# Optimization experiments

Hardware: AMD Instinct MI355X
Metric: run time of the kernel (lower is better)

Reference implementation:

```python
import jax, jax.numpy as jnp
import numpy as np
from jax import lax

NUM_MASKS = 100
NUM_CLASSES = 81  # 80 + 1
KERNEL_DIM = 256
BIAS_PRIOR = float(-np.log((1 - 0.01) / 0.01))


def setup_inputs() -> dict:
    key = jax.random.key(0)
    ks = jax.random.split(key, 12)
    B, C, H, W = 4, 256, 160, 160
    D = C  # expand_dim = in_channels * num_groups
    inp = {
        "features": jax.random.normal(ks[0], (B, C, H, W), jnp.float32),
        # iam_conv: Conv2d(C, num_masks, 3, padding=1)
        "w_iam": jax.random.normal(ks[1], (NUM_MASKS, C, 3, 3), jnp.float32) * 0.01,
        "b_iam": jnp.full((NUM_MASKS,), BIAS_PRIOR, jnp.float32),
        "softmax_bias": jnp.ones((1,), jnp.float32),
        # fc: Linear(D, D), xavier-ish
        "w_fc": jax.random.normal(ks[2], (D, D), jnp.float32) * (1.0 / np.sqrt(D)),
        "b_fc": jnp.zeros((D,), jnp.float32),
        "w_cls": jax.random.normal(ks[3], (NUM_CLASSES, D), jnp.float32) * 0.01,
        "b_cls": jnp.full((NUM_CLASSES,), BIAS_PRIOR, jnp.float32),
        "w_ker": jax.random.normal(ks[4], (KERNEL_DIM, D), jnp.float32) * 0.01,
        "b_ker": jnp.zeros((KERNEL_DIM,), jnp.float32),
        "w_obj": jax.random.normal(ks[5], (1, D), jnp.float32) * (1.0 / np.sqrt(D)),
        "b_obj": jnp.zeros((1,), jnp.float32),
        "w_box": jax.random.normal(ks[6], (4, D), jnp.float32) * 0.01,
        "b_box": jnp.zeros((4,), jnp.float32),
    }
    return inp


def reference(features, w_iam, b_iam, softmax_bias, w_fc, b_fc,
              w_cls, b_cls, w_ker, b_ker, w_obj, b_obj, w_box, b_box):
    B, C, H, W = features.shape
    # conv score map: (B, num_masks, H, W)
    iam = lax.conv_general_dilated(
        features, w_iam, window_strides=(1, 1), padding="SAME",
        dimension_numbers=("NCHW", "OIHW", "NCHW")) + b_iam[None, :, None, None]
    # num_groups == 1: single group iam
    iam_flat = iam.reshape(B, NUM_MASKS, H * W)
    # softmax over HW with learned scalar bias (bias shifts uniformly -> no-op math-wise but kept faithful)
    iam_prob = jax.nn.softmax(iam_flat + softmax_bias[0], axis=-1)  # (B, M, HW)
    # spatial attention pooling: bmm(prob, feats^T) -> (B, M, C)
    inst = jnp.einsum("bmp,bcp->bmc", iam_prob, features.reshape(B, C, H * W))
    # prev_inst_features is None -> skip fc_fuse
    inst = jax.nn.relu(inst @ w_fc.T + b_fc)
    pred_logits = inst @ w_cls.T + b_cls
    pred_kernel = inst @ w_ker.T + b_ker
    pred_scores = inst @ w_obj.T + b_obj
    pred_bboxes = inst @ w_box.T + b_box
    return (pred_logits, pred_kernel, pred_scores, pred_bboxes, iam, inst)
```

## Files before the change

kernel.cpp:

```cpp
#include <hip/hip_runtime.h>
#include <hip/hip_bf16.h>

typedef __attribute__((ext_vector_type(8))) short bf16x8;
typedef __attribute__((ext_vector_type(4))) float f32x4;

#define HW_ 25600
#define HP_ 162
#define WP_ 162

__device__ __forceinline__ unsigned short f2bf(float f) {
    union { float f; unsigned u; } x; x.f = f;
    unsigned r = x.u + 0x7FFFu + ((x.u >> 16) & 1u);
    return (unsigned short)(r >> 16);
}

typedef const __attribute__((address_space(1))) unsigned int* gas_t;
typedef __attribute__((address_space(3))) unsigned int* las_t;
__device__ __forceinline__ void gl_lds16(const void* g, void* l) {
    __builtin_amdgcn_global_load_lds((gas_t)g, (las_t)l, 16, 0, 0);
}

__global__ __launch_bounds__(256) void k_prepw(const float* __restrict__ w_iam,
                                               unsigned short* __restrict__ wp) {
    int idx = blockIdx.x * 256 + threadIdx.x;
    if (idx >= 36 * 8192) return;
    int stage = idx >> 13;
    int r8 = idx & 8191;
    int m = r8 >> 6, cl = r8 & 63;
    int tap = stage >> 2, cc = stage & 3;
    int c = cc * 64 + cl;
    int dy = tap / 3, dx = tap - dy * 3;
    float v = (m < 100) ? w_iam[((m * 256 + c) * 3 + dy) * 3 + dx] : 0.f;
    wp[idx] = f2bf(v);
}

__global__ __launch_bounds__(256) void k_border(unsigned short* __restrict__ fpad) {
    int idx = blockIdx.x * 256 + threadIdx.x;
    const int perb = 164864;
    if (idx >= 4 * perb) return;
    int b = idx / perb;
    int r = idx - b * perb;
    int hp, wpp, c;
    if (r < 82944) {
        hp = (r < 41472) ? 0 : 161;
        int r2 = r % 41472;
        wpp = r2 >> 8; c = r2 & 255;
    } else {
        r -= 82944;
        wpp = (r < 40960) ? 0 : 161;
        int r2 = r % 40960;
        hp = 1 + (r2 >> 8); c = r2 & 255;
    }
    fpad[((b * HP_ + hp) * WP_ + wpp) * 256 + c] = 0;
}

__global__ __launch_bounds__(256) void k_convert(const float* __restrict__ feat,
                                                 unsigned short* __restrict__ fpad) {
    int bid = blockIdx.x;
    int b = bid / 640;
    int h = (bid >> 2) % 160;
    int c0 = (bid & 3) * 64;
    __shared__ float tile[64][161];
    int t = threadIdx.x;
    const float* src = feat + ((long)(b * 256 + c0) * 160 + h) * 160;
    for (int s = 0; s < 40; ++s) {
        int q = t + s * 256;
        int ci = q / 160;
        int w = q - ci * 160;
        tile[ci][w] = src[(long)ci * HW_ + w];
    }
    __syncthreads();
    int co = (t & 7) * 8, wq = t >> 3;
    unsigned short* dst = fpad + ((long)(b * HP_ + h + 1) * WP_ + 1) * 256 + c0 + co;
    for (int wp = 0; wp < 5; ++wp) {
        int w = wq + wp * 32;
        bf16x8 v;
        #pragma unroll
        for (int j = 0; j < 8; ++j) v[j] = (short)f2bf(tile[co + j][w]);
        *(bf16x8*)(dst + (long)w * 256) = v;
    }
}

__global__ __launch_bounds__(256, 4) void k_conv(const unsigned short* __restrict__ fpad,
                                                 const unsigned short* __restrict__ wprep,
                                                 const float* __restrict__ b_iam,
                                                 float* __restrict__ iam) {
    int bid = blockIdx.x;
    bid = (bid & 7) * 100 + (bid >> 3);
    int b = bid / 200;
    int p0 = (bid % 200) * 128;
    int tid = threadIdx.x;
    int lane = tid & 63, wid = tid >> 6;

    __shared__ __align__(16) unsigned short As[128 * 64];
    __shared__ __align__(16) unsigned short Bs[128 * 64];

    const unsigned short* fb = fpad + (long)b * HP_ * WP_ * 256;
    const unsigned short* gB[4];
    #pragma unroll
    for (int rnd = 0; rnd < 4; ++rnd) {
        int r = (tid >> 3) + rnd * 32;
        int p = p0 + r;
        int h = p / 160, w = p - h * 160;
        gB[rnd] = fb + ((long)h * WP_ + w) * 256 + (tid & 7) * 8;
    }

    f32x4 acc[7][2];
    #pragma unroll
    for (int i = 0; i < 7; ++i)
        #pragma unroll
        for (int j = 0; j < 2; ++j)
            #pragma unroll
            for (int k = 0; k < 4; ++k) acc[i][j][k] = 0.f;

    int kgrp = (lane >> 4) << 3;
    int arow = lane & 15;

    for (int tap = 0; tap < 9; ++tap) {
        int dy = tap / 3, dx = tap - dy * 3;
        long toff = ((long)dy * WP_ + dx) * 256;
        #pragma unroll
        for (int cc = 0; cc < 4; ++cc) {
            int stage = tap * 4 + cc;
            const unsigned short* ga = wprep + (long)stage * 8192 + (tid << 3);
            long boff = toff + cc * 64;
            #pragma unroll
            for (int rnd = 0; rnd < 4; ++rnd) {
                gl_lds16(ga + rnd * 2048, (char*)As + (wid << 10) + (rnd << 12));
                gl_lds16(gB[rnd] + boff, (char*)Bs + (wid << 10) + (rnd << 12));
            }
            __syncthreads();
            #pragma unroll
            for (int kk = 0; kk < 64; kk += 32) {
                bf16x8 af[7], bfv[2];
                #pragma unroll
                for (int mf = 0; mf < 7; ++mf)
                    af[mf] = *(const bf16x8*)(As + (mf * 16 + arow) * 64 + kk + kgrp);
                #pragma unroll
                for (int nf = 0; nf < 2; ++nf)
                    bfv[nf] = *(const bf16x8*)(Bs + (wid * 32 + nf * 16 + arow) * 64 + kk + kgrp);
                #pragma unroll
                for (int mf = 0; mf < 7; ++mf)
                    #pragma unroll
                    for (int nf = 0; nf < 2; ++nf)
                        acc[mf][nf] = __builtin_amdgcn_mfma_f32_16x16x32_bf16(
                            af[mf], bfv[nf], acc[mf][nf], 0, 0, 0);
            }
            __syncthreads();
        }
    }
    float* dst = iam + (long)b * 100 * HW_;
    #pragma unroll
    for (int mf = 0; mf < 7; ++mf)
        #pragma unroll
        for (int nf = 0; nf < 2; ++nf) {
            int p = p0 + wid * 32 + nf * 16 + (lane & 15);
            int m0 = mf * 16 + ((lane >> 4) << 2);
            #pragma unroll
            for (int j = 0; j < 4; ++j) {
                int m = m0 + j;
                if (m < 100) dst[(long)m * HW_ + p] = acc[mf][nf][j] + b_iam[m];
            }
        }
}

__global__ __launch_bounds__(256, 2) void k_pool(const float* __restrict__ feat,
                                                 const float* __restrict__ iam,
                                                 float* __restrict__ partials,
                                                 float* __restrict__ psum) {
    int bid = blockIdx.x;
    int b = bid / 50;
    int slice = bid - b * 50;
    int p0 = slice * 512;
    int tid = threadIdx.x, lane = tid & 63, wq = tid >> 6;

    __shared__ __align__(16) unsigned short A[128 * 72];
    __shared__ __align__(16) unsigned short Bl[256 * 72];
    __shared__ float sums[128];
    if (tid < 128) sums[tid] = 0.f;
    __syncthreads();

    f32x4 acc[7][4];
    #pragma unroll
    for (int i = 0; i < 7; ++i)
        #pragma unroll
        for (int j = 0; j < 4; ++j)
            #pragma unroll
            for (int k = 0; k < 4; ++k) acc[i][j][k] = 0.f;

    int kgrp = (lane >> 4) << 3;

    for (int ks = 0; ks < 8; ++ks) {
        int k0 = p0 + ks * 64;
        for (int s = 0; s < 4; ++s) {
            int q = tid + s * 256;
            int mi = q >> 3, j0 = (q & 7) * 8;
            bf16x8 o;
            if (mi < 100) {
                const float4* sp4 = (const float4*)(iam + (long)(b * 100 + mi) * HW_ + k0 + j0);
                float4 v0 = sp4[0], v1 = sp4[1];
                float xv[8] = {v0.x, v0.y, v0.z, v0.w, v1.x, v1.y, v1.z, v1.w};
                float ls = 0.f;
                #pragma unroll
                for (int j = 0; j < 8; ++j) {
                    float e = __expf(xv[j]);
                    o[j] = (short)f2bf(e);
                    ls += e;
                }
                atomicAdd(&sums[mi], ls);
            } else {
                #pragma unroll
                for (int j = 0; j < 8; ++j) o[j] = 0;
            }
            *(bf16x8*)(A + mi * 72 + j0) = o;
        }
        for (int s = 0; s < 8; ++s) {
            int q = tid + s * 256;
            int ci = q >> 3, j0 = (q & 7) * 8;
            const float4* sp4 = (const float4*)(feat + (long)(b * 256 + ci) * HW_ + k0 + j0);
            float4 v0 = sp4[0], v1 = sp4[1];
            float xv[8] = {v0.x, v0.y, v0.z, v0.w, v1.x, v1.y, v1.z, v1.w};
            bf16x8 o;
            #pragma unroll
            for (int j = 0; j < 8; ++j) o[j] = (short)f2bf(xv[j]);
            *(bf16x8*)(Bl + ci * 72 + j0) = o;
        }
        __syncthreads();
        #pragma unroll
        for (int kk = 0; kk < 64; kk += 32) {
            bf16x8 af[7], bfv[4];
            #pragma unroll
            for (int mf = 0; mf < 7; ++mf)
                af[mf] = *(const bf16x8*)(A + (mf * 16 + (lane & 15)) * 72 + kk + kgrp);
            #pragma unroll
            for (int nf = 0; nf < 4; ++nf)
                bfv[nf] = *(const bf16x8*)(Bl + (wq * 64 + nf * 16 + (lane & 15)) * 72 + kk + kgrp);
            #pragma unroll
            for (int mf = 0; mf < 7; ++mf)
                #pragma unroll
                for (int nf = 0; nf < 4; ++nf)
                    acc[mf][nf] = __builtin_amdgcn_mfma_f32_16x16x32_bf16(
                        af[mf], bfv[nf], acc[mf][nf], 0, 0, 0);
        }
        __syncthreads();
    }
    if (tid < 100) psum[(long)(b * 50 + slice) * 112 + tid] = sums[tid];
    float* dst = partials + (long)(b * 50 + slice) * 112 * 256;
    #pragma unroll
    for (int mf = 0; mf < 7; ++mf)
        #pragma unroll
        for (int nf = 0; nf < 4; ++nf) {
            int m0 = mf * 16 + ((lane >> 4) << 2);
            int c  = wq * 64 + nf * 16 + (lane & 15);
            #pragma unroll
            for (int j = 0; j < 4; ++j)
                dst[(long)(m0 + j) * 256 + c] = acc[mf][nf][j];
        }
}

__global__ __launch_bounds__(256) void k_redpool(const float* __restrict__ partials,
                                                 const float* __restrict__ psum,
                                                 float* __restrict__ inst_pool) {
    int bid = blockIdx.x;
    int b = bid / 100, m = bid - b * 100;
    int c = threadIdx.x;
    float s = 0.f, d = 0.f;
    for (int sl = 0; sl < 50; ++sl) {
        s += partials[((long)(b * 50 + sl) * 112 + m) * 256 + c];
        d += psum[(long)(b * 50 + sl) * 112 + m];
    }
    inst_pool[(long)bid * 256 + c] = s / d;
}

__global__ __launch_bounds__(256) void k_fc(const float* __restrict__ inst_pool,
                                            const float* __restrict__ w_fc, const float* __restrict__ b_fc,
                                            const float* __restrict__ w_cls, const float* __restrict__ b_cls,
                                            const float* __restrict__ w_ker, const float* __restrict__ b_ker,
                                            const float* __restrict__ w_obj, const float* __restrict__ b_obj,
                                            const float* __restrict__ w_box, const float* __restrict__ b_box,
                                            float* __restrict__ out) {
    int r = blockIdx.x;
    int t = threadIdx.x;
    __shared__ float row[256];
    __shared__ float inst_s[256];
    row[t] = inst_pool[(long)r * 256 + t];
    __syncthreads();
    {
        float acc = b_fc[t];
        const float4* wv = (const float4*)(w_fc + (long)t * 256);
        for (int c = 0; c < 64; ++c) {
            float4 w4 = wv[c];
            acc += w4.x * row[c * 4] + w4.y * row[c * 4 + 1] + w4.z * row[c * 4 + 2] + w4.w * row[c * 4 + 3];
        }
        acc = fmaxf(acc, 0.f);
        inst_s[t] = acc;
        out[10376800 + (long)r * 256 + t] = acc;
    }
    __syncthreads();
    {
        float acc = b_ker[t];
        const float4* wv = (const float4*)(w_ker + (long)t * 256);
        for (int c = 0; c < 64; ++c) {
            float4 w4 = wv[c];
            acc += w4.x * inst_s[c * 4] + w4.y * inst_s[c * 4 + 1] + w4.z * inst_s[c * 4 + 2] + w4.w * inst_s[c * 4 + 3];
        }
        out[32400 + (long)r * 256 + t] = acc;
    }
    if (t < 81) {
        float acc = b_cls[t];
        const float4* wv = (const float4*)(w_cls + (long)t * 256);
        for (int c = 0; c < 64; ++c) {
            float4 w4 = wv[c];
            acc += w4.x * inst_s[c * 4] + w4.y * inst_s[c * 4 + 1] + w4.z * inst_s[c * 4 + 2] + w4.w * inst_s[c * 4 + 3];
        }
        out[(long)r * 81 + t] = acc;
    }
    if (t == 0) {
        float acc = b_obj[0];
        for (int c = 0; c < 256; ++c) acc += w_obj[c] * inst_s[c];
        out[134800 + r] = acc;
    }
    if (t >= 1 && t < 5) {
        int j = t - 1;
        float acc = b_box[j];
        for (int c = 0; c < 256; ++c) acc += w_box[j * 256 + c] * inst_s[c];
        out[135200 + (long)r * 4 + j] = acc;
    }
}

extern "C" void kernel_launch(void* const* d_in, const int* in_sizes, int n_in,
                              void* d_out, int out_size, void* d_ws, size_t ws_size,
                              hipStream_t stream) {
    const float* feat  = (const float*)d_in[0];
    const float* w_iam = (const float*)d_in[1];
    const float* b_iam = (const float*)d_in[2];
    const float* w_fc  = (const float*)d_in[4];
    const float* b_fc  = (const float*)d_in[5];
    const float* w_cls = (const float*)d_in[6];
    const float* b_cls = (const float*)d_in[7];
    const float* w_ker = (const float*)d_in[8];
    const float* b_ker = (const float*)d_in[9];
    const float* w_obj = (const float*)d_in[10];
    const float* b_obj = (const float*)d_in[11];
    const float* w_box = (const float*)d_in[12];
    const float* b_box = (const float*)d_in[13];
    float* out = (float*)d_out;

    char* ws = (char*)d_ws;
    unsigned short* fpad  = (unsigned short*)ws;
    unsigned short* wprep = (unsigned short*)(ws + 53747712);
    float* partials  = (float*)ws;
    float* psum      = (float*)(ws + 22937600);
    float* inst_pool = (float*)(ws + 23027200);

    float* iam = out + 136800;

    k_prepw  <<<dim3(1152), dim3(256), 0, stream>>>(w_iam, wprep);
    k_border <<<dim3(2576), dim3(256), 0, stream>>>(fpad);
    k_convert<<<dim3(2560), dim3(256), 0, stream>>>(feat, fpad);
    k_conv   <<<dim3(800),  dim3(256), 0, stream>>>(fpad, wprep, b_iam, iam);
    k_pool   <<<dim3(200),  dim3(256), 0, stream>>>(feat, iam, partials, psum);
    k_redpool<<<dim3(400),  dim3(256), 0, stream>>>(partials, psum, inst_pool);
    k_fc     <<<dim3(400),  dim3(256), 0, stream>>>(inst_pool, w_fc, b_fc, w_cls, b_cls,
                                                    w_ker, b_ker, w_obj, b_obj, w_box, b_box, out);
}
```

Measured before the change: 205.2 us.

## Double-buffer conv LDS stages and XOR-swizzle K chunks to avoid bank conflicts

The implicit-GEMM conv kernel gets two LDS buffers for A and B, so the async global_load_lds of stage s+2 is issued while stage s is computed, with explicit vmcnt waits and barriers. The weight prep and the feature-load addressing also XOR-swizzle 8-element channel groups by row, so the MFMA fragment reads from LDS avoid bank conflicts. LDS use doubles to 64KB per block and the occupancy hint of 4 blocks per CU is dropped, which lowers occupancy. The pipeline also relies on a hand-written vmcnt count being correct.

```diff
diff --git a/kernel.cpp b/kernel.cpp
--- a/kernel.cpp
+++ b/kernel.cpp
@@ -28,7 +28,8 @@
     int r8 = idx & 8191;
     int m = r8 >> 6, cl = r8 & 63;
     int tap = stage >> 2, cc = stage & 3;
-    int c = cc * 64 + cl;
+    int jj = (cl >> 3) ^ (m & 7);
+    int c = cc * 64 + jj * 8 + (cl & 7);
     int dy = tap / 3, dx = tap - dy * 3;
     float v = (m < 100) ? w_iam[((m * 256 + c) * 3 + dy) * 3 + dx] : 0.f;
     wp[idx] = f2bf(v);
@@ -81,10 +82,10 @@
     }
 }
 
-__global__ __launch_bounds__(256, 4) void k_conv(const unsigned short* __restrict__ fpad,
-                                                 const unsigned short* __restrict__ wprep,
-                                                 const float* __restrict__ b_iam,
-                                                 float* __restrict__ iam) {
+__global__ __launch_bounds__(256) void k_conv(const unsigned short* __restrict__ fpad,
+                                              const unsigned short* __restrict__ wprep,
+                                              const float* __restrict__ b_iam,
+                                              float* __restrict__ iam) {
     int bid = blockIdx.x;
     bid = (bid & 7) * 100 + (bid >> 3);
     int b = bid / 200;
@@ -92,18 +93,20 @@
     int tid = threadIdx.x;
     int lane = tid & 63, wid = tid >> 6;
 
-    __shared__ __align__(16) unsigned short As[128 * 64];
-    __shared__ __align__(16) unsigned short Bs[128 * 64];
+    __shared__ __align__(16) unsigned short As[2][8192];
+    __shared__ __align__(16) unsigned short Bs[2][8192];
 
     const unsigned short* fb = fpad + (long)b * HP_ * WP_ * 256;
     const unsigned short* gB[4];
+    int csw = (((tid & 7) ^ ((tid >> 3) & 7)) << 3);
     #pragma unroll
     for (int rnd = 0; rnd < 4; ++rnd) {
         int r = (tid >> 3) + rnd * 32;
         int p = p0 + r;
         int h = p / 160, w = p - h * 160;
-        gB[rnd] = fb + ((long)h * WP_ + w) * 256 + (tid & 7) * 8;
-    }
+        gB[rnd] = fb + ((long)h * WP_ + w) * 256 + csw;
+    }
+    const unsigned short* gA0 = wprep + (tid << 3);
 
     f32x4 acc[7][2];
     #pragma unroll
@@ -113,42 +116,65 @@
             #pragma unroll
             for (int k = 0; k < 4; ++k) acc[i][j][k] = 0.f;
 
-    int kgrp = (lane >> 4) << 3;
     int arow = lane & 15;
-
-    for (int tap = 0; tap < 9; ++tap) {
+    int cs0 = ((((lane >> 4) ^ (lane & 7))) << 3);
+    int cs1 = cs0 ^ 32;
+
+    auto issue = [&](int s, int bi) {
+        int tap = s >> 2, cc = s & 3;
         int dy = tap / 3, dx = tap - dy * 3;
-        long toff = ((long)dy * WP_ + dx) * 256;
-        #pragma unroll
-        for (int cc = 0; cc < 4; ++cc) {
-            int stage = tap * 4 + cc;
-            const unsigned short* ga = wprep + (long)stage * 8192 + (tid << 3);
-            long boff = toff + cc * 64;
-            #pragma unroll
-            for (int rnd = 0; rnd < 4; ++rnd) {
-                gl_lds16(ga + rnd * 2048, (char*)As + (wid << 10) + (rnd << 12));
-                gl_lds16(gB[rnd] + boff, (char*)Bs + (wid << 10) + (rnd << 12));
-            }
-            __syncthreads();
-            #pragma unroll
-            for (int kk = 0; kk < 64; kk += 32) {
-                bf16x8 af[7], bfv[2];
-                #pragma unroll
-                for (int mf = 0; mf < 7; ++mf)
-                    af[mf] = *(const bf16x8*)(As + (mf * 16 + arow) * 64 + kk + kgrp);
+        long boff = ((long)dy * WP_ + dx) * 256 + cc * 64;
+        const unsigned short* ga = gA0 + ((long)s << 13);
+        char* Ad = (char*)As[bi];
+        char* Bd = (char*)Bs[bi];
+        #pragma unroll
+        for (int rnd = 0; rnd < 4; ++rnd) {
+            gl_lds16(ga + (rnd << 11), Ad + (wid << 10) + (rnd << 12));
+            gl_lds16(gB[rnd] + boff,   Bd + (wid << 10) + (rnd << 12));
+        }
+    };
+
+    auto compute = [&](int bi) {
+        const unsigned short* Ab = As[bi];
+        const unsigned short* Bb = Bs[bi];
+        #pragma unroll
+        for (int kk = 0; kk < 2; ++kk) {
+            int co = kk ? cs1 : cs0;
+            bf16x8 af[7], bfv[2];
+            #pragma unroll
+            for (int mf = 0; mf < 7; ++mf)
+                af[mf] = *(const bf16x8*)(Ab + (mf * 16 + arow) * 64 + co);
+            #pragma unroll
+            for (int nf = 0; nf < 2; ++nf)
+                bfv[nf] = *(const bf16x8*)(Bb + (wid * 32 + nf * 16 + arow) * 64 + co);
+            #pragma unroll
+            for (int mf = 0; mf < 7; ++mf)
                 #pragma unroll
                 for (int nf = 0; nf < 2; ++nf)
-                    bfv[nf] = *(const bf16x8*)(Bs + (wid * 32 + nf * 16 + arow) * 64 + kk + kgrp);
-                #pragma unroll
-                for (int mf = 0; mf < 7; ++mf)
-                    #pragma unroll
-                    for (int nf = 0; nf < 2; ++nf)
-                        acc[mf][nf] = __builtin_amdgcn_mfma_f32_16x16x32_bf16(
-                            af[mf], bfv[nf], acc[mf][nf], 0, 0, 0);
-            }
-            __syncthreads();
-        }
-    }
+                    acc[mf][nf] = __builtin_amdgcn_mfma_f32_16x16x32_bf16(
+                        af[mf], bfv[nf], acc[mf][nf], 0, 0, 0);
+        }
+    };
+
+    issue(0, 0);
+    issue(1, 1);
+    for (int s = 0; s < 35; ++s) {
+        asm volatile("s_waitcnt vmcnt(8)" ::: "memory");
+        __builtin_amdgcn_sched_barrier(0);
+        __builtin_amdgcn_s_barrier();
+        __builtin_amdgcn_sched_barrier(0);
+        compute(s & 1);
+        __builtin_amdgcn_sched_barrier(0);
+        __builtin_amdgcn_s_barrier();
+        __builtin_amdgcn_sched_barrier(0);
+        if (s < 34) issue(s + 2, s & 1);
+    }
+    asm volatile("s_waitcnt vmcnt(0)" ::: "memory");
+    __builtin_amdgcn_sched_barrier(0);
+    __builtin_amdgcn_s_barrier();
+    __builtin_amdgcn_sched_barrier(0);
+    compute(1);
+
     float* dst = iam + (long)b * 100 * HW_;
     #pragma unroll
     for (int mf = 0; mf < 7; ++mf)
```

After: 201.5 us. About the same (-1.8%).
